# Kernel optimization log

Measured on AMD Instinct MI355X. Metric: run time of the kernel, lower is better.

Reference implementation:

```python
import jax, jax.numpy as jnp
import numpy as np

B, N, L, D, H = 32, 512, 1024, 512, 8
C = D // H  # 64 channels per head
SCALE = C ** -0.5


def setup_inputs() -> dict:
    key = jax.random.key(0)
    ks = jax.random.split(key, 10)
    inp = {
        "x_q": jax.random.normal(ks[0], (B, N, D), dtype=jnp.float32),
        "x_kv": jax.random.normal(ks[1], (B, L, D), dtype=jnp.float32),
        "pad_mask": jax.random.randint(ks[2], (B, L), 0, 2).astype(bool),
        # projection weights stored (in, out); no bias except o_proj
        "Wq": jax.random.normal(ks[3], (D, D), dtype=jnp.float32) * (D ** -0.5),
        "Wk": jax.random.normal(ks[4], (D, D), dtype=jnp.float32) * (D ** -0.5),
        "Wv": jax.random.normal(ks[5], (D, D), dtype=jnp.float32) * (D ** -0.5),
        "Wo": jax.random.normal(ks[6], (D, D), dtype=jnp.float32) * (D ** -0.5),
        "bo": jnp.zeros((D,), dtype=jnp.float32),
        # relative position bias, shape (1, feat_w*feat_h, num_qk_channels)
        "rpb": jax.random.normal(ks[7], (1, L, D), dtype=jnp.float32) * 0.02,
    }
    return inp


def reference(x_q, x_kv, pad_mask, Wq, Wk, Wv, Wo, bo, rpb):
    # linear projections
    q = jnp.einsum("bnd,de->bne", x_q, Wq)
    k = jnp.einsum("bld,de->ble", x_kv, Wk) + rpb  # rel-pos bias added to K
    v = jnp.einsum("bld,de->ble", x_kv, Wv)
    # split heads: (B, S, H*C) -> (B, H, S, C)
    split = lambda t: t.reshape(t.shape[0], t.shape[1], H, C).transpose(0, 2, 1, 3)
    q, k, v = split(q), split(k), split(v)
    attn = jnp.einsum("bhic,bhjc->bhij", q, k) * SCALE  # (B,H,N,L)
    neg = -jnp.finfo(attn.dtype).max
    attn = jnp.where(pad_mask[:, None, None, :], neg, attn)
    attn = jax.nn.softmax(attn, axis=-1)
    o = jnp.einsum("bhij,bhjc->bhic", attn, v)
    o = o.transpose(0, 2, 1, 3).reshape(B, N, H * C)  # merge heads
    return jnp.einsum("bnd,de->bne", o, Wo) + bo
```

## Files before the change

kernel.cpp:

```cpp
#include <hip/hip_runtime.h>
#include <hip/hip_bf16.h>

typedef __hip_bfloat16 bf16;
typedef __attribute__((ext_vector_type(8))) short short8;
typedef __attribute__((ext_vector_type(4))) float f32x4;
typedef __attribute__((ext_vector_type(16))) float f32x16;

#define B_SZ 32
#define N_SZ 512
#define L_SZ 1024
#define D_SZ 512
#define H_SZ 8

__device__ __forceinline__ void gload16(void* lds, const void* g) {
    typedef const __attribute__((address_space(1))) unsigned int* gp_t;
    typedef __attribute__((address_space(3))) unsigned int* lp_t;
    __builtin_amdgcn_global_load_lds((gp_t)g, (lp_t)lds, 16, 0, 0);
}

__device__ __forceinline__ unsigned int cvtpk(float lo, float hi) {
    unsigned int r;
    asm("v_cvt_pk_bf16_f32 %0, %1, %2" : "=v"(r) : "v"(lo), "v"(hi));
    return r;
}

__device__ __forceinline__ float fexp2(float x) {
    float r;
    asm("v_exp_f32 %0, %1" : "=v"(r) : "v"(x));
    return r;
}

struct alignas(8) B4 { bf16 a, b, c, d; };

__global__ void cvt_all(const float* __restrict__ xq, const float* __restrict__ xkv,
                        bf16* __restrict__ dq, bf16* __restrict__ dkv) {
    int i = blockIdx.x * 256 + threadIdx.x;
    const float* s;
    bf16* d;
    if (i < 2097152) {
        s = xq; d = dq;
    } else {
        i -= 2097152; s = xkv; d = dkv;
    }
    float4 v = ((const float4*)s)[i];
    B4 o;
    o.a = __float2bfloat16(v.x);
    o.b = __float2bfloat16(v.y);
    o.c = __float2bfloat16(v.z);
    o.d = __float2bfloat16(v.w);
    *(B4*)(d + (size_t)i * 4) = o;
}

__global__ void tpose4(const float* __restrict__ s0, const float* __restrict__ s1,
                       const float* __restrict__ s2, const float* __restrict__ s3,
                       bf16* __restrict__ d0, bf16* __restrict__ d1,
                       bf16* __restrict__ d2, bf16* __restrict__ d3) {
    __shared__ float t[32][33];
    const float* s = blockIdx.z == 0 ? s0 : blockIdx.z == 1 ? s1 : blockIdx.z == 2 ? s2 : s3;
    bf16* d = blockIdx.z == 0 ? d0 : blockIdx.z == 1 ? d1 : blockIdx.z == 2 ? d2 : d3;
    int tx = threadIdx.x, ty = threadIdx.y;
    int r0 = blockIdx.y * 32, c0 = blockIdx.x * 32;
#pragma unroll
    for (int i = 0; i < 32; i += 8)
        t[ty + i][tx] = s[(size_t)(r0 + ty + i) * 512 + c0 + tx];
    __syncthreads();
#pragma unroll
    for (int i = 0; i < 32; i += 8)
        d[(size_t)(c0 + ty + i) * 512 + r0 + tx] = __float2bfloat16(t[tx][ty + i]);
}

__global__ __launch_bounds__(256) void gemm_qkv(
    const bf16* __restrict__ xq, const bf16* __restrict__ xkv,
    const bf16* __restrict__ WqT, const bf16* __restrict__ WkT,
    const bf16* __restrict__ WvT, const float* __restrict__ rpb,
    bf16* __restrict__ qh, bf16* __restrict__ kh, bf16* __restrict__ vTh) {
    __shared__ char sm[2][32768];
    const int tid = threadIdx.x;
    const int wave = tid >> 6, lane = tid & 63;
    const int wr = wave >> 1, wc = wave & 1;
    const int g16 = lane >> 4, r16 = lane & 15;

    const int orig = blockIdx.x;
    const int bid = (orig & 7) * 320 + (orig >> 3);

    int mode;
    long rowBase;
    int colBase;
    const bf16 *A, *Bt;
    if (bid < 512) {
        mode = 0; A = xq; Bt = WqT;
        rowBase = (long)(bid >> 2) * 128; colBase = (bid & 3) * 128;
    } else if (bid < 1536) {
        mode = 1; int t = bid - 512; A = xkv; Bt = WkT;
        rowBase = (long)(t >> 2) * 128; colBase = (t & 3) * 128;
    } else {
        mode = 2; int t = bid - 1536; A = WvT; Bt = xkv;
        rowBase = (long)(t & 3) * 128; colBase = (t >> 2) * 128;
    }

    const int row_ = tid >> 3;
    const int gj_ = ((tid & 7) ^ (row_ & 7)) * 8;
    const bf16* aSrc = A + (rowBase + row_) * 512 + gj_;
    const bf16* bSrc = Bt + ((long)colBase + row_) * 512 + gj_;

    f32x4 acc[4][4];
#pragma unroll
    for (int m = 0; m < 4; ++m)
#pragma unroll
        for (int n = 0; n < 4; ++n) acc[m][n] = {0.f, 0.f, 0.f, 0.f};

#pragma unroll
    for (int rnd = 0; rnd < 4; ++rnd) {
        gload16(&sm[0][rnd * 4096 + tid * 16], aSrc + rnd * 16384);
        gload16(&sm[0][16384 + rnd * 4096 + tid * 16], bSrc + rnd * 16384);
    }
    __syncthreads();

    for (int t = 0; t < 8; ++t) {
        const int cur = t & 1;
        if (t < 7) {
            const int nk = (t + 1) * 64;
#pragma unroll
            for (int rnd = 0; rnd < 4; ++rnd) {
                gload16(&sm[cur ^ 1][rnd * 4096 + tid * 16], aSrc + rnd * 16384 + nk);
                gload16(&sm[cur ^ 1][16384 + rnd * 4096 + tid * 16], bSrc + rnd * 16384 + nk);
            }
        }
        const char* lA = &sm[cur][0];
        const char* lB = &sm[cur][16384];
#pragma unroll
        for (int kk = 0; kk < 2; ++kk) {
            short8 a[4], b[4];
#pragma unroll
            for (int m = 0; m < 4; ++m) {
                int row = wr * 64 + m * 16 + r16;
                a[m] = *(const short8*)(lA + row * 128 + (((kk * 4 + g16) ^ (row & 7)) * 16));
            }
#pragma unroll
            for (int n = 0; n < 4; ++n) {
                int row = wc * 64 + n * 16 + r16;
                b[n] = *(const short8*)(lB + row * 128 + (((kk * 4 + g16) ^ (row & 7)) * 16));
            }
#pragma unroll
            for (int m = 0; m < 4; ++m)
#pragma unroll
                for (int n = 0; n < 4; ++n)
                    acc[m][n] =
                        __builtin_amdgcn_mfma_f32_16x16x32_bf16(a[m], b[n], acc[m][n], 0, 0, 0);
        }
        __syncthreads();
    }

    float* ep = (float*)((char*)sm + wave * 16384);
#pragma unroll
    for (int m = 0; m < 4; ++m)
#pragma unroll
        for (int n = 0; n < 4; ++n)
#pragma unroll
            for (int r = 0; r < 4; ++r)
                ep[(m * 16 + g16 * 4 + r) * 64 + n * 16 + r16] = acc[m][n][r];

    const long gm0 = rowBase + wr * 64;
    const int e0 = colBase + wc * 64;
    bf16* obase;
    int rstride;
    int s0g = 0;
    if (mode == 2) {
        int hh = (int)gm0 >> 6;
        int bb = e0 >> 10, s0 = e0 & 1023;
        obase = vTh + (((long)bb * H_SZ + hh) * 64 + ((int)gm0 & 63)) * (long)L_SZ + s0;
        rstride = L_SZ;
    } else if (mode == 1) {
        int bb = (int)(gm0 >> 10), s0 = (int)gm0 & 1023;
        int hh = e0 >> 6;
        obase = kh + (((long)bb * H_SZ + hh) * (long)L_SZ + s0) * 64 + (e0 & 63);
        rstride = 64;
        s0g = (int)gm0 & 1023;
    } else {
        int bb = (int)(gm0 >> 9), s0 = (int)gm0 & 511;
        int hh = e0 >> 6;
        obase = qh + (((long)bb * H_SZ + hh) * (long)N_SZ + s0) * 64 + (e0 & 63);
        rstride = 64;
    }

#pragma unroll
    for (int i = 0; i < 8; ++i) {
        int chunk = i * 64 + lane;
        int lr = chunk >> 3, cc = chunk & 7;
        float4 fa = *(float4*)(ep + lr * 64 + cc * 8);
        float4 fb = *(float4*)(ep + lr * 64 + cc * 8 + 4);
        if (mode == 1) {
            const float* rp = rpb + (long)(s0g + lr) * 512 + e0 + cc * 8;
            float4 ra = *(const float4*)rp;
            float4 rb = *(const float4*)(rp + 4);
            fa.x += ra.x; fa.y += ra.y; fa.z += ra.z; fa.w += ra.w;
            fb.x += rb.x; fb.y += rb.y; fb.z += rb.z; fb.w += rb.w;
        }
        uint4 st;
        st.x = cvtpk(fa.x, fa.y);
        st.y = cvtpk(fa.z, fa.w);
        st.z = cvtpk(fb.x, fb.y);
        st.w = cvtpk(fb.z, fb.w);
        *(uint4*)(obase + (long)lr * rstride + cc * 8) = st;
    }
}

__global__ __launch_bounds__(256) void gemm_o(const bf16* __restrict__ A,
                                              const bf16* __restrict__ Bt,
                                              float* __restrict__ outp,
                                              const float* __restrict__ bias) {
    __shared__ char sm[2][32768];
    const int tid = threadIdx.x;
    const int wave = tid >> 6, lane = tid & 63;
    const int wr = wave >> 1, wc = wave & 1;
    const int g16 = lane >> 4, r16 = lane & 15;

    const int orig = blockIdx.x;
    const int bid = (orig & 7) * 64 + (orig >> 3);
    const long rowBase = (long)(bid >> 2) * 128;
    const int colBase = (bid & 3) * 128;

    const int row_ = tid >> 3;
    const int gj_ = ((tid & 7) ^ (row_ & 7)) * 8;
    const bf16* aSrc = A + (rowBase + row_) * 512 + gj_;
    const bf16* bSrc = Bt + ((long)colBase + row_) * 512 + gj_;

    f32x4 acc[4][4];
#pragma unroll
    for (int m = 0; m < 4; ++m)
#pragma unroll
        for (int n = 0; n < 4; ++n) acc[m][n] = {0.f, 0.f, 0.f, 0.f};

#pragma unroll
    for (int rnd = 0; rnd < 4; ++rnd) {
        gload16(&sm[0][rnd * 4096 + tid * 16], aSrc + rnd * 16384);
        gload16(&sm[0][16384 + rnd * 4096 + tid * 16], bSrc + rnd * 16384);
    }
    __syncthreads();

    for (int t = 0; t < 8; ++t) {
        const int cur = t & 1;
        if (t < 7) {
            const int nk = (t + 1) * 64;
#pragma unroll
            for (int rnd = 0; rnd < 4; ++rnd) {
                gload16(&sm[cur ^ 1][rnd * 4096 + tid * 16], aSrc + rnd * 16384 + nk);
                gload16(&sm[cur ^ 1][16384 + rnd * 4096 + tid * 16], bSrc + rnd * 16384 + nk);
            }
        }
        const char* lA = &sm[cur][0];
        const char* lB = &sm[cur][16384];
#pragma unroll
        for (int kk = 0; kk < 2; ++kk) {
            short8 a[4], b[4];
#pragma unroll
            for (int m = 0; m < 4; ++m) {
                int row = wr * 64 + m * 16 + r16;
                a[m] = *(const short8*)(lA + row * 128 + (((kk * 4 + g16) ^ (row & 7)) * 16));
            }
#pragma unroll
            for (int n = 0; n < 4; ++n) {
                int row = wc * 64 + n * 16 + r16;
                b[n] = *(const short8*)(lB + row * 128 + (((kk * 4 + g16) ^ (row & 7)) * 16));
            }
#pragma unroll
            for (int m = 0; m < 4; ++m)
#pragma unroll
                for (int n = 0; n < 4; ++n)
                    acc[m][n] =
                        __builtin_amdgcn_mfma_f32_16x16x32_bf16(a[m], b[n], acc[m][n], 0, 0, 0);
        }
        __syncthreads();
    }

#pragma unroll
    for (int m = 0; m < 4; ++m) {
#pragma unroll
        for (int r = 0; r < 4; ++r) {
            long gm = rowBase + wr * 64 + m * 16 + g16 * 4 + r;
#pragma unroll
            for (int n = 0; n < 4; ++n) {
                int e = colBase + wc * 64 + n * 16 + r16;
                outp[gm * 512 + e] = acc[m][n][r] + bias[e];
            }
        }
    }
}

__global__ __launch_bounds__(512, 4) void attn256(const bf16* __restrict__ q,
                                                  const bf16* __restrict__ k,
                                                  const bf16* __restrict__ vT,
                                                  const int* __restrict__ mask,
                                                  bf16* __restrict__ o) {
    __shared__ bf16 lK[2][64 * 64];
    __shared__ bf16 lV[2][64 * 64];
    __shared__ float lMf[1024];

    const int tid = threadIdx.x;
    const int wv = tid >> 6, lane = tid & 63;
    const int q32 = lane & 31, hi = lane >> 5;

    const int wg = blockIdx.x;
    const int xcd = wg & 7, slot = wg >> 3;
    const int bh = xcd * 32 + (slot >> 1), qc = slot & 1;
    const int b = bh >> 3, h = bh & 7;

    const bf16* kbase = k + (long)bh * L_SZ * 64;
    const bf16* vbase = vT + (long)bh * 64 * L_SZ;

    const int* mrow = mask + b * L_SZ;
    lMf[tid] = mrow[tid] ? -1e38f : 0.f;
    lMf[tid + 512] = mrow[tid + 512] ? -1e38f : 0.f;

    const int r_ = tid >> 3, j_ = tid & 7;
    const int gj_ = (j_ ^ (r_ & 7)) * 8;
    const bf16* gK = kbase + r_ * 64 + gj_;
    const bf16* gV = vbase + (long)r_ * L_SZ + gj_;
    char* dK0 = (char*)(&lK[0][0]) + tid * 16;
    char* dK1 = (char*)(&lK[1][0]) + tid * 16;
    char* dV0 = (char*)(&lV[0][0]) + tid * 16;
    char* dV1 = (char*)(&lV[1][0]) + tid * 16;
    gload16(dK0, gK);
    gload16(dV0, gV);

    const bf16* qp = q + ((long)bh * N_SZ + qc * 256 + wv * 32 + q32) * 64 + hi * 8;
    short8 qf[4];
#pragma unroll
    for (int t = 0; t < 4; ++t) qf[t] = *(const short8*)(qp + t * 16);

    float mrun = 0.f, lrun = 0.f;
    f32x16 oa0, oa1;
#pragma unroll
    for (int i = 0; i < 16; ++i) { oa0[i] = 0.f; oa1[i] = 0.f; }

    __syncthreads();

    const float CL = 0.18033688011112042f;

    for (int kb = 0; kb < 16; ++kb) {
        const char* curK = (const char*)(&lK[kb & 1][0]);
        const char* curV = (const char*)(&lV[kb & 1][0]);
        if (kb < 15) {
            gload16((kb & 1) ? dK0 : dK1, gK + (kb + 1) * 4096);
            gload16((kb & 1) ? dV0 : dV1, gV + (kb + 1) * 64);
        }

        f32x16 sA, sB;
#pragma unroll
        for (int i = 0; i < 16; ++i) { sA[i] = 0.f; sB[i] = 0.f; }
#pragma unroll
        for (int t = 0; t < 4; ++t) {
            int sl = ((t * 2 + hi) ^ (q32 & 7)) * 16;
            short8 kfA = *(const short8*)(curK + q32 * 128 + sl);
            short8 kfB = *(const short8*)(curK + (32 + q32) * 128 + sl);
            sA = __builtin_amdgcn_mfma_f32_32x32x16_bf16(kfA, qf[t], sA, 0, 0, 0);
            sB = __builtin_amdgcn_mfma_f32_32x32x16_bf16(kfB, qf[t], sB, 0, 0, 0);
        }

        const float* mf = lMf + kb * 64 + hi * 4;
        float4 ma0 = *(const float4*)(mf);
        float4 ma1 = *(const float4*)(mf + 8);
        float4 ma2 = *(const float4*)(mf + 16);
        float4 ma3 = *(const float4*)(mf + 24);
        float4 mb0 = *(const float4*)(mf + 32);
        float4 mb1 = *(const float4*)(mf + 40);
        float4 mb2 = *(const float4*)(mf + 48);
        float4 mb3 = *(const float4*)(mf + 56);
        float mba[16] = {ma0.x, ma0.y, ma0.z, ma0.w, ma1.x, ma1.y, ma1.z, ma1.w,
                         ma2.x, ma2.y, ma2.z, ma2.w, ma3.x, ma3.y, ma3.z, ma3.w};
        float mbb[16] = {mb0.x, mb0.y, mb0.z, mb0.w, mb1.x, mb1.y, mb1.z, mb1.w,
                         mb2.x, mb2.y, mb2.z, mb2.w, mb3.x, mb3.y, mb3.z, mb3.w};

        float t32[32];
#pragma unroll
        for (int i = 0; i < 16; ++i) {
            t32[i] = fmaf(sA[i], CL, mba[i]);
            t32[16 + i] = fmaf(sB[i], CL, mbb[i]);
        }

        float m16[16];
#pragma unroll
        for (int i = 0; i < 16; ++i) m16[i] = fmaxf(t32[i], t32[16 + i]);
        float m8[8];
#pragma unroll
        for (int i = 0; i < 8; ++i) m8[i] = fmaxf(m16[i], m16[i + 8]);
        float tm = fmaxf(fmaxf(fmaxf(m8[0], m8[4]), fmaxf(m8[1], m8[5])),
                         fmaxf(fmaxf(m8[2], m8[6]), fmaxf(m8[3], m8[7])));
        tm = fmaxf(tm, __shfl_xor(tm, 32));

        if (__any(tm > mrun + 8.f)) {
            float mnew = fmaxf(mrun, tm);
            float al = fexp2(mrun - mnew);
            mrun = mnew;
            lrun *= al;
#pragma unroll
            for (int i = 0; i < 16; ++i) { oa0[i] *= al; oa1[i] *= al; }
        }

#pragma unroll
        for (int i = 0; i < 32; ++i) t32[i] = fexp2(t32[i] - mrun);
        float s16[16];
#pragma unroll
        for (int i = 0; i < 16; ++i) s16[i] = t32[i] + t32[16 + i];
        float s8[8];
#pragma unroll
        for (int i = 0; i < 8; ++i) s8[i] = s16[i] + s16[i + 8];
        float ps = ((s8[0] + s8[4]) + (s8[1] + s8[5])) + ((s8[2] + s8[6]) + (s8[3] + s8[7]));
        ps += __shfl_xor(ps, 32);
        lrun += ps;

        union U { unsigned int u[4]; short8 s8v; };
        U fr[4];
#pragma unroll
        for (int fkt = 0; fkt < 4; ++fkt) {
            const float* tp = t32 + fkt * 8;
            unsigned int y0 = cvtpk(tp[0], tp[1]);
            unsigned int y1 = cvtpk(tp[2], tp[3]);
            unsigned int y2 = cvtpk(tp[4], tp[5]);
            unsigned int y3 = cvtpk(tp[6], tp[7]);
            asm("v_permlane32_swap_b32 %0, %1" : "+v"(y0), "+v"(y2));
            asm("v_permlane32_swap_b32 %0, %1" : "+v"(y1), "+v"(y3));
            fr[fkt].u[0] = y0; fr[fkt].u[1] = y1; fr[fkt].u[2] = y2; fr[fkt].u[3] = y3;
        }

#pragma unroll
        for (int kt = 0; kt < 4; ++kt) {
            int sw = ((kt * 2 + hi) ^ (q32 & 7)) * 16;
            short8 v0 = *(const short8*)(curV + q32 * 128 + sw);
            short8 v1 = *(const short8*)(curV + (32 + q32) * 128 + sw);
            oa0 = __builtin_amdgcn_mfma_f32_32x32x16_bf16(v0, fr[kt].s8v, oa0, 0, 0, 0);
            oa1 = __builtin_amdgcn_mfma_f32_32x32x16_bf16(v1, fr[kt].s8v, oa1, 0, 0, 0);
        }

        __syncthreads();
    }

    float inv = 1.f / lrun;
    bf16* op = o + ((long)b * N_SZ + qc * 256 + wv * 32 + q32) * 512 + h * 64;
#pragma unroll
    for (int ct = 0; ct < 2; ++ct) {
#pragma unroll
        for (int rq = 0; rq < 4; ++rq) {
            int c0 = ct * 32 + rq * 8 + hi * 4;
            float v0 = (ct ? oa1[rq * 4 + 0] : oa0[rq * 4 + 0]) * inv;
            float v1 = (ct ? oa1[rq * 4 + 1] : oa0[rq * 4 + 1]) * inv;
            float v2 = (ct ? oa1[rq * 4 + 2] : oa0[rq * 4 + 2]) * inv;
            float v3 = (ct ? oa1[rq * 4 + 3] : oa0[rq * 4 + 3]) * inv;
            uint2 st;
            st.x = cvtpk(v0, v1);
            st.y = cvtpk(v2, v3);
            *(uint2*)(op + c0) = st;
        }
    }
}

extern "C" void kernel_launch(void* const* d_in, const int* in_sizes, int n_in,
                              void* d_out, int out_size, void* d_ws, size_t ws_size,
                              hipStream_t stream) {
    const float* x_q  = (const float*)d_in[0];
    const float* x_kv = (const float*)d_in[1];
    const int*   mask = (const int*)d_in[2];
    const float* Wq   = (const float*)d_in[3];
    const float* Wk   = (const float*)d_in[4];
    const float* Wv   = (const float*)d_in[5];
    const float* Wo   = (const float*)d_in[6];
    const float* bo   = (const float*)d_in[7];
    const float* rpb  = (const float*)d_in[8];
    float* out = (float*)d_out;

    char* w = (char*)d_ws;
    bf16* xq_bf  = (bf16*)(w + 0);
    bf16* xkv_bf = (bf16*)(w + 16777216);
    bf16* WqT    = (bf16*)(w + 50331648);
    bf16* WkT    = WqT + 262144;
    bf16* WvT    = WkT + 262144;
    bf16* WoT    = WvT + 262144;
    bf16* qh     = (bf16*)(w + 52428800);
    bf16* kh     = (bf16*)(w + 69206016);
    bf16* vTh    = (bf16*)(w + 102760448);
    bf16* o_bf   = xq_bf;

    cvt_all<<<24576, 256, 0, stream>>>(x_q, x_kv, xq_bf, xkv_bf);
    tpose4<<<dim3(16, 16, 4), dim3(32, 8), 0, stream>>>(Wq, Wk, Wv, Wo, WqT, WkT, WvT, WoT);

    gemm_qkv<<<2560, 256, 0, stream>>>(xq_bf, xkv_bf, WqT, WkT, WvT, rpb, qh, kh, vTh);

    attn256<<<512, 512, 0, stream>>>(qh, kh, vTh, mask, o_bf);

    gemm_o<<<512, 256, 0, stream>>>(o_bf, WoT, out, bo);
}
```

Before: 164.4 us.

## Stage GEMM tiles through registers with single LDS buffer to raise occupancy

```diff
diff --git a/kernel.cpp b/kernel.cpp
--- a/kernel.cpp
+++ b/kernel.cpp
@@ -28,6 +28,12 @@
     float r;
     asm("v_exp_f32 %0, %1" : "=v"(r) : "v"(x));
     return r;
+}
+
+__device__ __forceinline__ void bar_lgkm() {
+    asm volatile("s_waitcnt lgkmcnt(0)" ::: "memory");
+    __builtin_amdgcn_s_barrier();
+    asm volatile("" ::: "memory");
 }
 
 struct alignas(8) B4 { bf16 a, b, c, d; };
@@ -69,12 +75,12 @@
         d[(size_t)(c0 + ty + i) * 512 + r0 + tx] = __float2bfloat16(t[tx][ty + i]);
 }
 
-__global__ __launch_bounds__(256) void gemm_qkv(
+__global__ __launch_bounds__(256, 4) void gemm_qkv(
     const bf16* __restrict__ xq, const bf16* __restrict__ xkv,
     const bf16* __restrict__ WqT, const bf16* __restrict__ WkT,
     const bf16* __restrict__ WvT, const float* __restrict__ rpb,
     bf16* __restrict__ qh, bf16* __restrict__ kh, bf16* __restrict__ vTh) {
-    __shared__ char sm[2][32768];
+    __shared__ char sm[32768];
     const int tid = threadIdx.x;
     const int wave = tid >> 6, lane = tid & 63;
     const int wr = wave >> 1, wc = wave & 1;
@@ -109,37 +115,38 @@
 #pragma unroll
         for (int n = 0; n < 4; ++n) acc[m][n] = {0.f, 0.f, 0.f, 0.f};
 
-#pragma unroll
-    for (int rnd = 0; rnd < 4; ++rnd) {
-        gload16(&sm[0][rnd * 4096 + tid * 16], aSrc + rnd * 16384);
-        gload16(&sm[0][16384 + rnd * 4096 + tid * 16], bSrc + rnd * 16384);
-    }
-    __syncthreads();
+    uint4 ra[4], rb[4];
+#pragma unroll
+    for (int r = 0; r < 4; ++r) {
+        ra[r] = *(const uint4*)(aSrc + r * 16384);
+        rb[r] = *(const uint4*)(bSrc + r * 16384);
+    }
+#pragma unroll
+    for (int r = 0; r < 4; ++r) {
+        *(uint4*)&sm[r * 4096 + tid * 16] = ra[r];
+        *(uint4*)&sm[16384 + r * 4096 + tid * 16] = rb[r];
+    }
+#pragma unroll
+    for (int r = 0; r < 4; ++r) {
+        ra[r] = *(const uint4*)(aSrc + r * 16384 + 64);
+        rb[r] = *(const uint4*)(bSrc + r * 16384 + 64);
+    }
+    bar_lgkm();
 
     for (int t = 0; t < 8; ++t) {
-        const int cur = t & 1;
-        if (t < 7) {
-            const int nk = (t + 1) * 64;
-#pragma unroll
-            for (int rnd = 0; rnd < 4; ++rnd) {
-                gload16(&sm[cur ^ 1][rnd * 4096 + tid * 16], aSrc + rnd * 16384 + nk);
-                gload16(&sm[cur ^ 1][16384 + rnd * 4096 + tid * 16], bSrc + rnd * 16384 + nk);
-            }
-        }
-        const char* lA = &sm[cur][0];
-        const char* lB = &sm[cur][16384];
 #pragma unroll
         for (int kk = 0; kk < 2; ++kk) {
             short8 a[4], b[4];
 #pragma unroll
             for (int m = 0; m < 4; ++m) {
                 int row = wr * 64 + m * 16 + r16;
-                a[m] = *(const short8*)(lA + row * 128 + (((kk * 4 + g16) ^ (row & 7)) * 16));
+                a[m] = *(const short8*)(&sm[row * 128 + (((kk * 4 + g16) ^ (row & 7)) * 16)]);
             }
 #pragma unroll
             for (int n = 0; n < 4; ++n) {
                 int row = wc * 64 + n * 16 + r16;
-                b[n] = *(const short8*)(lB + row * 128 + (((kk * 4 + g16) ^ (row & 7)) * 16));
+                b[n] = *(const short8*)(
+                    &sm[16384 + row * 128 + (((kk * 4 + g16) ^ (row & 7)) * 16)]);
             }
 #pragma unroll
             for (int m = 0; m < 4; ++m)
@@ -148,18 +155,28 @@
                     acc[m][n] =
                         __builtin_amdgcn_mfma_f32_16x16x32_bf16(a[m], b[n], acc[m][n], 0, 0, 0);
         }
-        __syncthreads();
-    }
-
-    float* ep = (float*)((char*)sm + wave * 16384);
-#pragma unroll
-    for (int m = 0; m < 4; ++m)
-#pragma unroll
-        for (int n = 0; n < 4; ++n)
-#pragma unroll
-            for (int r = 0; r < 4; ++r)
-                ep[(m * 16 + g16 * 4 + r) * 64 + n * 16 + r16] = acc[m][n][r];
-
+        if (t < 7) {
+            bar_lgkm();
+#pragma unroll
+            for (int r = 0; r < 4; ++r) {
+                *(uint4*)&sm[r * 4096 + tid * 16] = ra[r];
+                *(uint4*)&sm[16384 + r * 4096 + tid * 16] = rb[r];
+            }
+            if (t < 6) {
+                const int nk = (t + 2) * 64;
+#pragma unroll
+                for (int r = 0; r < 4; ++r) {
+                    ra[r] = *(const uint4*)(aSrc + r * 16384 + nk);
+                    rb[r] = *(const uint4*)(bSrc + r * 16384 + nk);
+                }
+            }
+            bar_lgkm();
+        }
+    }
+
+    __syncthreads();
+
+    float* ep = (float*)(sm + wave * 8192);
     const long gm0 = rowBase + wr * 64;
     const int e0 = colBase + wc * 64;
     bf16* obase;
@@ -184,32 +201,46 @@
     }
 
 #pragma unroll
-    for (int i = 0; i < 8; ++i) {
-        int chunk = i * 64 + lane;
-        int lr = chunk >> 3, cc = chunk & 7;
-        float4 fa = *(float4*)(ep + lr * 64 + cc * 8);
-        float4 fb = *(float4*)(ep + lr * 64 + cc * 8 + 4);
-        if (mode == 1) {
-            const float* rp = rpb + (long)(s0g + lr) * 512 + e0 + cc * 8;
-            float4 ra = *(const float4*)rp;
-            float4 rb = *(const float4*)(rp + 4);
-            fa.x += ra.x; fa.y += ra.y; fa.z += ra.z; fa.w += ra.w;
-            fb.x += rb.x; fb.y += rb.y; fb.z += rb.z; fb.w += rb.w;
-        }
-        uint4 st;
-        st.x = cvtpk(fa.x, fa.y);
-        st.y = cvtpk(fa.z, fa.w);
-        st.z = cvtpk(fb.x, fb.y);
-        st.w = cvtpk(fb.z, fb.w);
-        *(uint4*)(obase + (long)lr * rstride + cc * 8) = st;
-    }
-}
-
-__global__ __launch_bounds__(256) void gemm_o(const bf16* __restrict__ A,
-                                              const bf16* __restrict__ Bt,
-                                              float* __restrict__ outp,
-                                              const float* __restrict__ bias) {
-    __shared__ char sm[2][32768];
+    for (int half = 0; half < 2; ++half) {
+#pragma unroll
+        for (int dm = 0; dm < 2; ++dm) {
+            int m = half * 2 + dm;
+#pragma unroll
+            for (int n = 0; n < 4; ++n)
+#pragma unroll
+                for (int r = 0; r < 4; ++r)
+                    ep[(dm * 16 + g16 * 4 + r) * 64 + n * 16 + r16] = acc[m][n][r];
+        }
+#pragma unroll
+        for (int i = 0; i < 4; ++i) {
+            int chunk = i * 64 + lane;
+            int lr = chunk >> 3, cc = chunk & 7;
+            float4 fa = *(float4*)(ep + lr * 64 + cc * 8);
+            float4 fb = *(float4*)(ep + lr * 64 + cc * 8 + 4);
+            int grow = half * 32 + lr;
+            if (mode == 1) {
+                const float* rp = rpb + (long)(s0g + grow) * 512 + e0 + cc * 8;
+                float4 rra = *(const float4*)rp;
+                float4 rrb = *(const float4*)(rp + 4);
+                fa.x += rra.x; fa.y += rra.y; fa.z += rra.z; fa.w += rra.w;
+                fb.x += rrb.x; fb.y += rrb.y; fb.z += rrb.z; fb.w += rrb.w;
+            }
+            uint4 st;
+            st.x = cvtpk(fa.x, fa.y);
+            st.y = cvtpk(fa.z, fa.w);
+            st.z = cvtpk(fb.x, fb.y);
+            st.w = cvtpk(fb.z, fb.w);
+            *(uint4*)(obase + (long)grow * rstride + cc * 8) = st;
+        }
+        asm volatile("" ::: "memory");
+    }
+}
+
+__global__ __launch_bounds__(256, 4) void gemm_o(const bf16* __restrict__ A,
+                                                 const bf16* __restrict__ Bt,
+                                                 float* __restrict__ outp,
+                                                 const float* __restrict__ bias) {
+    __shared__ char sm[32768];
     const int tid = threadIdx.x;
     const int wave = tid >> 6, lane = tid & 63;
     const int wr = wave >> 1, wc = wave & 1;
@@ -231,37 +262,38 @@
 #pragma unroll
         for (int n = 0; n < 4; ++n) acc[m][n] = {0.f, 0.f, 0.f, 0.f};
 
-#pragma unroll
-    for (int rnd = 0; rnd < 4; ++rnd) {
-        gload16(&sm[0][rnd * 4096 + tid * 16], aSrc + rnd * 16384);
-        gload16(&sm[0][16384 + rnd * 4096 + tid * 16], bSrc + rnd * 16384);
-    }
-    __syncthreads();
+    uint4 ra[4], rb[4];
+#pragma unroll
+    for (int r = 0; r < 4; ++r) {
+        ra[r] = *(const uint4*)(aSrc + r * 16384);
+        rb[r] = *(const uint4*)(bSrc + r * 16384);
+    }
+#pragma unroll
+    for (int r = 0; r < 4; ++r) {
+        *(uint4*)&sm[r * 4096 + tid * 16] = ra[r];
+        *(uint4*)&sm[16384 + r * 4096 + tid * 16] = rb[r];
+    }
+#pragma unroll
+    for (int r = 0; r < 4; ++r) {
+        ra[r] = *(const uint4*)(aSrc + r * 16384 + 64);
+        rb[r] = *(const uint4*)(bSrc + r * 16384 + 64);
+    }
+    bar_lgkm();
 
     for (int t = 0; t < 8; ++t) {
-        const int cur = t & 1;
-        if (t < 7) {
-            const int nk = (t + 1) * 64;
-#pragma unroll
-            for (int rnd = 0; rnd < 4; ++rnd) {
-                gload16(&sm[cur ^ 1][rnd * 4096 + tid * 16], aSrc + rnd * 16384 + nk);
-                gload16(&sm[cur ^ 1][16384 + rnd * 4096 + tid * 16], bSrc + rnd * 16384 + nk);
-            }
-        }
-        const char* lA = &sm[cur][0];
-        const char* lB = &sm[cur][16384];
 #pragma unroll
         for (int kk = 0; kk < 2; ++kk) {
             short8 a[4], b[4];
 #pragma unroll
             for (int m = 0; m < 4; ++m) {
                 int row = wr * 64 + m * 16 + r16;
-                a[m] = *(const short8*)(lA + row * 128 + (((kk * 4 + g16) ^ (row & 7)) * 16));
+                a[m] = *(const short8*)(&sm[row * 128 + (((kk * 4 + g16) ^ (row & 7)) * 16)]);
             }
 #pragma unroll
             for (int n = 0; n < 4; ++n) {
                 int row = wc * 64 + n * 16 + r16;
-                b[n] = *(const short8*)(lB + row * 128 + (((kk * 4 + g16) ^ (row & 7)) * 16));
+                b[n] = *(const short8*)(
+                    &sm[16384 + row * 128 + (((kk * 4 + g16) ^ (row & 7)) * 16)]);
             }
 #pragma unroll
             for (int m = 0; m < 4; ++m)
@@ -270,7 +302,23 @@
                     acc[m][n] =
                         __builtin_amdgcn_mfma_f32_16x16x32_bf16(a[m], b[n], acc[m][n], 0, 0, 0);
         }
-        __syncthreads();
+        if (t < 7) {
+            bar_lgkm();
+#pragma unroll
+            for (int r = 0; r < 4; ++r) {
+                *(uint4*)&sm[r * 4096 + tid * 16] = ra[r];
+                *(uint4*)&sm[16384 + r * 4096 + tid * 16] = rb[r];
+            }
+            if (t < 6) {
+                const int nk = (t + 2) * 64;
+#pragma unroll
+                for (int r = 0; r < 4; ++r) {
+                    ra[r] = *(const uint4*)(aSrc + r * 16384 + nk);
+                    rb[r] = *(const uint4*)(bSrc + r * 16384 + nk);
+                }
+            }
+            bar_lgkm();
+        }
     }
 
 #pragma unroll
```

Result: slower. 281.8 us (+71.5%).

## Fuse fp32-to-bf16 activation conversion into QKV GEMM and shrink LDS tiles

Applied to the files above, without the earlier changes.

```diff
diff --git a/kernel.cpp b/kernel.cpp
--- a/kernel.cpp
+++ b/kernel.cpp
@@ -28,27 +28,6 @@
     float r;
     asm("v_exp_f32 %0, %1" : "=v"(r) : "v"(x));
     return r;
-}
-
-struct alignas(8) B4 { bf16 a, b, c, d; };
-
-__global__ void cvt_all(const float* __restrict__ xq, const float* __restrict__ xkv,
-                        bf16* __restrict__ dq, bf16* __restrict__ dkv) {
-    int i = blockIdx.x * 256 + threadIdx.x;
-    const float* s;
-    bf16* d;
-    if (i < 2097152) {
-        s = xq; d = dq;
-    } else {
-        i -= 2097152; s = xkv; d = dkv;
-    }
-    float4 v = ((const float4*)s)[i];
-    B4 o;
-    o.a = __float2bfloat16(v.x);
-    o.b = __float2bfloat16(v.y);
-    o.c = __float2bfloat16(v.z);
-    o.d = __float2bfloat16(v.w);
-    *(B4*)(d + (size_t)i * 4) = o;
 }
 
 __global__ void tpose4(const float* __restrict__ s0, const float* __restrict__ s1,
@@ -70,11 +49,11 @@
 }
 
 __global__ __launch_bounds__(256) void gemm_qkv(
-    const bf16* __restrict__ xq, const bf16* __restrict__ xkv,
+    const float* __restrict__ xq, const float* __restrict__ xkv,
     const bf16* __restrict__ WqT, const bf16* __restrict__ WkT,
     const bf16* __restrict__ WvT, const float* __restrict__ rpb,
     bf16* __restrict__ qh, bf16* __restrict__ kh, bf16* __restrict__ vTh) {
-    __shared__ char sm[2][32768];
+    __shared__ char sm[32768];
     const int tid = threadIdx.x;
     const int wave = tid >> 6, lane = tid & 63;
     const int wr = wave >> 1, wc = wave & 1;
@@ -83,25 +62,34 @@
     const int orig = blockIdx.x;
     const int bid = (orig & 7) * 320 + (orig >> 3);
 
-    int mode;
+    int mode, xIsA;
     long rowBase;
     int colBase;
-    const bf16 *A, *Bt;
+    const float* X;
+    const bf16* W;
     if (bid < 512) {
-        mode = 0; A = xq; Bt = WqT;
+        mode = 0; X = xq; W = WqT; xIsA = 1;
         rowBase = (long)(bid >> 2) * 128; colBase = (bid & 3) * 128;
     } else if (bid < 1536) {
-        mode = 1; int t = bid - 512; A = xkv; Bt = WkT;
+        int t = bid - 512;
+        mode = 1; X = xkv; W = WkT; xIsA = 1;
         rowBase = (long)(t >> 2) * 128; colBase = (t & 3) * 128;
     } else {
-        mode = 2; int t = bid - 1536; A = WvT; Bt = xkv;
+        int t = bid - 1536;
+        mode = 2; X = xkv; W = WvT; xIsA = 0;
         rowBase = (long)(t & 3) * 128; colBase = (t >> 2) * 128;
     }
-
-    const int row_ = tid >> 3;
-    const int gj_ = ((tid & 7) ^ (row_ & 7)) * 8;
-    const bf16* aSrc = A + (rowBase + row_) * 512 + gj_;
-    const bf16* bSrc = Bt + ((long)colBase + row_) * 512 + gj_;
+    const long xBase = xIsA ? rowBase : (long)colBase;
+    const long wBase = xIsA ? (long)colBase : rowBase;
+    const int xsel = xIsA ? wr : wc;
+    const int wsel = xIsA ? wc : wr;
+
+    const int xrow = tid >> 3;
+    const int xcol = ((tid & 7) ^ (xrow & 7)) * 4;
+    const float* xSrc = X + (xBase + xrow) * 512 + xcol;
+    const int wrow = tid >> 2;
+    const int wcol = ((tid & 3) ^ (wrow & 3)) * 8;
+    const bf16* wSrc = W + (wBase + wrow) * 512 + wcol;
 
     f32x4 acc[4][4];
 #pragma unroll
@@ -109,57 +97,54 @@
 #pragma unroll
         for (int n = 0; n < 4; ++n) acc[m][n] = {0.f, 0.f, 0.f, 0.f};
 
-#pragma unroll
-    for (int rnd = 0; rnd < 4; ++rnd) {
-        gload16(&sm[0][rnd * 4096 + tid * 16], aSrc + rnd * 16384);
-        gload16(&sm[0][16384 + rnd * 4096 + tid * 16], bSrc + rnd * 16384);
-    }
-    __syncthreads();
-
-    for (int t = 0; t < 8; ++t) {
-        const int cur = t & 1;
-        if (t < 7) {
-            const int nk = (t + 1) * 64;
-#pragma unroll
-            for (int rnd = 0; rnd < 4; ++rnd) {
-                gload16(&sm[cur ^ 1][rnd * 4096 + tid * 16], aSrc + rnd * 16384 + nk);
-                gload16(&sm[cur ^ 1][16384 + rnd * 4096 + tid * 16], bSrc + rnd * 16384 + nk);
-            }
-        }
-        const char* lA = &sm[cur][0];
-        const char* lB = &sm[cur][16384];
-#pragma unroll
-        for (int kk = 0; kk < 2; ++kk) {
-            short8 a[4], b[4];
-#pragma unroll
-            for (int m = 0; m < 4; ++m) {
-                int row = wr * 64 + m * 16 + r16;
-                a[m] = *(const short8*)(lA + row * 128 + (((kk * 4 + g16) ^ (row & 7)) * 16));
-            }
-#pragma unroll
-            for (int n = 0; n < 4; ++n) {
-                int row = wc * 64 + n * 16 + r16;
-                b[n] = *(const short8*)(lB + row * 128 + (((kk * 4 + g16) ^ (row & 7)) * 16));
-            }
+    for (int t = 0; t < 16; ++t) {
+        const int k0 = t * 32;
+#pragma unroll
+        for (int rnd = 0; rnd < 4; ++rnd)
+            gload16(&sm[(rnd * 256 + tid) * 16], xSrc + rnd * 32 * 512 + k0);
+#pragma unroll
+        for (int rnd = 0; rnd < 2; ++rnd)
+            gload16(&sm[16384 + (rnd * 256 + tid) * 16], wSrc + rnd * 64 * 512 + k0);
+        __syncthreads();
+
+        short8 xf[4], wf[4];
+#pragma unroll
+        for (int i = 0; i < 4; ++i) {
+            int row = xsel * 64 + i * 16 + r16;
+            const char* rp = &sm[row * 128];
+            float4 qa = *(const float4*)(rp + (((2 * g16) ^ (row & 7)) * 16));
+            float4 qb = *(const float4*)(rp + (((2 * g16 + 1) ^ (row & 7)) * 16));
+            union { unsigned int u[4]; short8 s; } f;
+            f.u[0] = cvtpk(qa.x, qa.y);
+            f.u[1] = cvtpk(qa.z, qa.w);
+            f.u[2] = cvtpk(qb.x, qb.y);
+            f.u[3] = cvtpk(qb.z, qb.w);
+            xf[i] = f.s;
+        }
+#pragma unroll
+        for (int i = 0; i < 4; ++i) {
+            int row = wsel * 64 + i * 16 + r16;
+            wf[i] = *(const short8*)(&sm[16384 + row * 64 + ((g16 ^ (row & 3)) * 16)]);
+        }
+        if (xIsA) {
 #pragma unroll
             for (int m = 0; m < 4; ++m)
 #pragma unroll
                 for (int n = 0; n < 4; ++n)
                     acc[m][n] =
-                        __builtin_amdgcn_mfma_f32_16x16x32_bf16(a[m], b[n], acc[m][n], 0, 0, 0);
+                        __builtin_amdgcn_mfma_f32_16x16x32_bf16(xf[m], wf[n], acc[m][n], 0, 0, 0);
+        } else {
+#pragma unroll
+            for (int m = 0; m < 4; ++m)
+#pragma unroll
+                for (int n = 0; n < 4; ++n)
+                    acc[m][n] =
+                        __builtin_amdgcn_mfma_f32_16x16x32_bf16(wf[m], xf[n], acc[m][n], 0, 0, 0);
         }
         __syncthreads();
     }
 
-    float* ep = (float*)((char*)sm + wave * 16384);
-#pragma unroll
-    for (int m = 0; m < 4; ++m)
-#pragma unroll
-        for (int n = 0; n < 4; ++n)
-#pragma unroll
-            for (int r = 0; r < 4; ++r)
-                ep[(m * 16 + g16 * 4 + r) * 64 + n * 16 + r16] = acc[m][n][r];
-
+    float* ep = (float*)(sm + wave * 8192);
     const long gm0 = rowBase + wr * 64;
     const int e0 = colBase + wc * 64;
     bf16* obase;
@@ -184,24 +169,38 @@
     }
 
 #pragma unroll
-    for (int i = 0; i < 8; ++i) {
-        int chunk = i * 64 + lane;
-        int lr = chunk >> 3, cc = chunk & 7;
-        float4 fa = *(float4*)(ep + lr * 64 + cc * 8);
-        float4 fb = *(float4*)(ep + lr * 64 + cc * 8 + 4);
-        if (mode == 1) {
-            const float* rp = rpb + (long)(s0g + lr) * 512 + e0 + cc * 8;
-            float4 ra = *(const float4*)rp;
-            float4 rb = *(const float4*)(rp + 4);
-            fa.x += ra.x; fa.y += ra.y; fa.z += ra.z; fa.w += ra.w;
-            fb.x += rb.x; fb.y += rb.y; fb.z += rb.z; fb.w += rb.w;
-        }
-        uint4 st;
-        st.x = cvtpk(fa.x, fa.y);
-        st.y = cvtpk(fa.z, fa.w);
-        st.z = cvtpk(fb.x, fb.y);
-        st.w = cvtpk(fb.z, fb.w);
-        *(uint4*)(obase + (long)lr * rstride + cc * 8) = st;
+    for (int half = 0; half < 2; ++half) {
+#pragma unroll
+        for (int dm = 0; dm < 2; ++dm) {
+            int m = half * 2 + dm;
+#pragma unroll
+            for (int n = 0; n < 4; ++n)
+#pragma unroll
+                for (int r = 0; r < 4; ++r)
+                    ep[(dm * 16 + g16 * 4 + r) * 64 + n * 16 + r16] = acc[m][n][r];
+        }
+#pragma unroll
+        for (int i = 0; i < 4; ++i) {
+            int chunk = i * 64 + lane;
+            int lr = chunk >> 3, cc = chunk & 7;
+            float4 fa = *(float4*)(ep + lr * 64 + cc * 8);
+            float4 fb = *(float4*)(ep + lr * 64 + cc * 8 + 4);
+            int grow = half * 32 + lr;
+            if (mode == 1) {
+                const float* rp = rpb + (long)(s0g + grow) * 512 + e0 + cc * 8;
+                float4 rra = *(const float4*)rp;
+                float4 rrb = *(const float4*)(rp + 4);
+                fa.x += rra.x; fa.y += rra.y; fa.z += rra.z; fa.w += rra.w;
+                fb.x += rrb.x; fb.y += rrb.y; fb.z += rrb.z; fb.w += rrb.w;
+            }
+            uint4 st;
+            st.x = cvtpk(fa.x, fa.y);
+            st.y = cvtpk(fa.z, fa.w);
+            st.z = cvtpk(fb.x, fb.y);
+            st.w = cvtpk(fb.z, fb.w);
+            *(uint4*)(obase + (long)grow * rstride + cc * 8) = st;
+        }
+        asm volatile("" ::: "memory");
     }
 }
 
@@ -209,7 +208,7 @@
                                               const bf16* __restrict__ Bt,
                                               float* __restrict__ outp,
                                               const float* __restrict__ bias) {
-    __shared__ char sm[2][32768];
+    __shared__ char sm[16384];
     const int tid = threadIdx.x;
     const int wave = tid >> 6, lane = tid & 63;
     const int wr = wave >> 1, wc = wave & 1;
@@ -220,8 +219,8 @@
     const long rowBase = (long)(bid >> 2) * 128;
     const int colBase = (bid & 3) * 128;
 
-    const int row_ = tid >> 3;
-    const int gj_ = ((tid & 7) ^ (row_ & 7)) * 8;
+    const int row_ = tid >> 2;
+    const int gj_ = ((tid & 3) ^ (row_ & 3)) * 8;
     const bf16* aSrc = A + (rowBase + row_) * 512 + gj_;
     const bf16* bSrc = Bt + ((long)colBase + row_) * 512 + gj_;
 
@@ -231,45 +230,31 @@
 #pragma unroll
         for (int n = 0; n < 4; ++n) acc[m][n] = {0.f, 0.f, 0.f, 0.f};
 
-#pragma unroll
-    for (int rnd = 0; rnd < 4; ++rnd) {
-        gload16(&sm[0][rnd * 4096 + tid * 16], aSrc + rnd * 16384);
-        gload16(&sm[0][16384 + rnd * 4096 + tid * 16], bSrc + rnd * 16384);
-    }
-    __syncthreads();
-
-    for (int t = 0; t < 8; ++t) {
-        const int cur = t & 1;
-        if (t < 7) {
-            const int nk = (t + 1) * 64;
-#pragma unroll
-            for (int rnd = 0; rnd < 4; ++rnd) {
-                gload16(&sm[cur ^ 1][rnd * 4096 + tid * 16], aSrc + rnd * 16384 + nk);
-                gload16(&sm[cur ^ 1][16384 + rnd * 4096 + tid * 16], bSrc + rnd * 16384 + nk);
-            }
-        }
-        const char* lA = &sm[cur][0];
-        const char* lB = &sm[cur][16384];
-#pragma unroll
-        for (int kk = 0; kk < 2; ++kk) {
-            short8 a[4], b[4];
-#pragma unroll
-            for (int m = 0; m < 4; ++m) {
-                int row = wr * 64 + m * 16 + r16;
-                a[m] = *(const short8*)(lA + row * 128 + (((kk * 4 + g16) ^ (row & 7)) * 16));
-            }
-#pragma unroll
-            for (int n = 0; n < 4; ++n) {
-                int row = wc * 64 + n * 16 + r16;
-                b[n] = *(const short8*)(lB + row * 128 + (((kk * 4 + g16) ^ (row & 7)) * 16));
-            }
-#pragma unroll
-            for (int m = 0; m < 4; ++m)
-#pragma unroll
-                for (int n = 0; n < 4; ++n)
-                    acc[m][n] =
-                        __builtin_amdgcn_mfma_f32_16x16x32_bf16(a[m], b[n], acc[m][n], 0, 0, 0);
-        }
+    for (int t = 0; t < 16; ++t) {
+        const int k0 = t * 32;
+#pragma unroll
+        for (int rnd = 0; rnd < 2; ++rnd) {
+            gload16(&sm[(rnd * 256 + tid) * 16], aSrc + rnd * 64 * 512 + k0);
+            gload16(&sm[8192 + (rnd * 256 + tid) * 16], bSrc + rnd * 64 * 512 + k0);
+        }
+        __syncthreads();
+        short8 a[4], b[4];
+#pragma unroll
+        for (int m = 0; m < 4; ++m) {
+            int row = wr * 64 + m * 16 + r16;
+            a[m] = *(const short8*)(&sm[row * 64 + ((g16 ^ (row & 3)) * 16)]);
+        }
+#pragma unroll
+        for (int n = 0; n < 4; ++n) {
+            int row = wc * 64 + n * 16 + r16;
+            b[n] = *(const short8*)(&sm[8192 + row * 64 + ((g16 ^ (row & 3)) * 16)]);
+        }
+#pragma unroll
+        for (int m = 0; m < 4; ++m)
+#pragma unroll
+            for (int n = 0; n < 4; ++n)
+                acc[m][n] =
+                    __builtin_amdgcn_mfma_f32_16x16x32_bf16(a[m], b[n], acc[m][n], 0, 0, 0);
         __syncthreads();
     }
 
@@ -469,8 +454,7 @@
     float* out = (float*)d_out;
 
     char* w = (char*)d_ws;
-    bf16* xq_bf  = (bf16*)(w + 0);
-    bf16* xkv_bf = (bf16*)(w + 16777216);
+    bf16* o_bf   = (bf16*)(w + 0);
     bf16* WqT    = (bf16*)(w + 50331648);
     bf16* WkT    = WqT + 262144;
     bf16* WvT    = WkT + 262144;
@@ -478,12 +462,10 @@
     bf16* qh     = (bf16*)(w + 52428800);
     bf16* kh     = (bf16*)(w + 69206016);
     bf16* vTh    = (bf16*)(w + 102760448);
-    bf16* o_bf   = xq_bf;
-
-    cvt_all<<<24576, 256, 0, stream>>>(x_q, x_kv, xq_bf, xkv_bf);
+
     tpose4<<<dim3(16, 16, 4), dim3(32, 8), 0, stream>>>(Wq, Wk, Wv, Wo, WqT, WkT, WvT, WoT);
 
-    gemm_qkv<<<2560, 256, 0, stream>>>(xq_bf, xkv_bf, WqT, WkT, WvT, rpb, qh, kh, vTh);
+    gemm_qkv<<<2560, 256, 0, stream>>>(x_q, x_kv, WqT, WkT, WvT, rpb, qh, kh, vTh);
 
     attn256<<<512, 512, 0, stream>>>(qh, kh, vTh, mask, o_bf);
 
```

Measured after the change: 179.6 us. +9.3%, slower.
